# Kernel tuning notes

Measured on AMD Instinct MI355X. Metric: run time of the kernel, lower is better.

The kernel has to match this reference:

```python
import jax, jax.numpy as jnp
import numpy as np

B, C, H, W = 16, 1536, 32, 32
M = 64      # num_clusters
L = 128     # cluster_dim
G = 256     # token_dim
HID = 512
OT_ITERS = 3
EPS = 1e-6


def setup_inputs() -> dict:
    key = jax.random.key(0)
    ks = jax.random.split(key, 12)
    def w(k, shape, fan_in):
        return jax.random.normal(k, shape, jnp.float32) * (1.0 / np.sqrt(fan_in))
    return {
        'x': jax.random.normal(ks[0], (B, C, H, W), jnp.float32),
        't': jax.random.normal(ks[1], (B, C), jnp.float32),
        # token_features: Linear(C->512), ReLU, Linear(512->G)
        'Wt1': w(ks[2], (HID, C), C), 'bt1': jnp.zeros((HID,), jnp.float32),
        'Wt2': w(ks[3], (G, HID), HID), 'bt2': jnp.zeros((G,), jnp.float32),
        # cluster_features: 1x1 Conv(C->512), ReLU, 1x1 Conv(512->L)
        'Wc1': w(ks[4], (HID, C), C), 'bc1': jnp.zeros((HID,), jnp.float32),
        'Wc2': w(ks[5], (L, HID), HID), 'bc2': jnp.zeros((L,), jnp.float32),
        # score: 1x1 Conv(C->512), ReLU, 1x1 Conv(512->M)
        'Ws1': w(ks[6], (HID, C), C), 'bs1': jnp.zeros((HID,), jnp.float32),
        'Ws2': w(ks[7], (M, HID), HID), 'bs2': jnp.zeros((M,), jnp.float32),
        # temp_predictor: Conv1d(L->1, k=1)
        'Wtp': w(ks[8], (L,), L), 'btp': jnp.zeros((), jnp.float32),
        'dust_bin': jnp.asarray(1.0, jnp.float32),
        'burst_b': jnp.asarray(0.0, jnp.float32),
        'burst_p': jnp.asarray(1.0, jnp.float32),
        'lambda_discount': jnp.asarray(0.5, jnp.float32),
    }


def _log_optimal_transport(scores, alpha, iters):
    # scores: [B, m, n]; alpha: scalar dust-bin logit
    b, m, n = scores.shape
    Z0 = jnp.concatenate([scores, jnp.broadcast_to(alpha, (b, 1, n))], axis=1)  # [B, m+1, n]
    norm = -jnp.log(jnp.asarray(m + n, scores.dtype))
    log_mu = jnp.concatenate([jnp.full((m,), norm, scores.dtype),
                              (jnp.log(jnp.asarray(n, scores.dtype)) + norm)[None]])  # [m+1]
    log_nu = jnp.full((n,), norm, scores.dtype)
    u = jnp.zeros((b, m + 1), scores.dtype)
    v = jnp.zeros((b, n), scores.dtype)
    for _ in range(iters):
        u = log_mu - jax.nn.logsumexp(Z0 + v[:, None, :], axis=2)
        v = log_nu - jax.nn.logsumexp(Z0 + u[:, :, None], axis=1)
    return Z0 + u[:, :, None] + v[:, None, :] - norm


def _l2norm(a, axis):
    return a / jnp.maximum(jnp.linalg.norm(a, axis=axis, keepdims=True), 1e-12)


def _forward(x, t, Wt1, bt1, Wt2, bt2, Wc1, bc1, Wc2, bc2, Ws1, bs1, Ws2, bs2,
             Wtp, btp, dust_bin, burst_b, burst_p, lambda_discount):
    b, c, h, w = x.shape
    n = h * w
    xf = x.reshape(b, c, n)  # [B, C, N] (1x1 convs == per-pixel MLP)
    # cluster features f: [B, L, N]
    h1 = jax.nn.relu(jnp.einsum('bcn,oc->bon', xf, Wc1) + bc1[:, None])
    f = jnp.einsum('bhn,lh->bln', h1, Wc2) + bc2[:, None]
    # assignment scores p: [B, M, N]
    h2 = jax.nn.relu(jnp.einsum('bcn,oc->bon', xf, Ws1) + bs1[:, None])
    p = jnp.einsum('bhn,mh->bmn', h2, Ws2) + bs2[:, None]
    # global token: [B, G]
    tok = jax.nn.relu(t @ Wt1.T + bt1) @ Wt2.T + bt2
    # Sinkhorn OT soft assignment, drop dust bin row
    P = jnp.exp(_log_optimal_transport(p, dust_bin, OT_ITERS))[:, :-1, :]  # [B, M, N]
    # burst-aware weighting
    f_norm = _l2norm(f, axis=1)                                  # [B, L, N]
    T_i = jax.nn.softplus(jnp.einsum('bln,l->bn', f, Wtp) + btp)  # [B, N]
    sim = jnp.einsum('bli,blj->bij', f_norm, f_norm)              # [B, N, N]
    T_avg = (T_i[:, :, None] + T_i[:, None, :]) * 0.5
    burst_w = jax.nn.sigmoid(T_avg * sim + burst_b)
    discount = jnp.clip(jnp.sum(burst_w, axis=-1) ** burst_p, 1e-3, 1e3)  # [B, N]
    lam = jax.nn.sigmoid(lambda_discount)
    P_adj = (1.0 - lam) * P + lam * (P / (discount[:, None, :] + EPS))
    # local aggregation: (f[:, :, None, :] * P[:, None, :, :]).sum(-1) == batched matmul
    agg = jnp.einsum('bln,bmn->blm', f, P_adj)  # [B, L, M]
    agg = _l2norm(agg, axis=1).reshape(b, -1)   # [B, L*M]
    tok_n = _l2norm(tok, axis=-1)
    g = jnp.concatenate([tok_n, agg], axis=-1)  # [B, G + L*M]
    return _l2norm(g, axis=-1)


def reference(x, t, Wt1, bt1, Wt2, bt2, Wc1, bc1, Wc2, bc2, Ws1, bs1, Ws2, bs2,
              Wtp, btp, dust_bin, burst_b, burst_p, lambda_discount):
    return _forward(x, t, Wt1, bt1, Wt2, bt2, Wc1, bc1, Wc2, bc2, Ws1, bs1, Ws2, bs2,
                    Wtp, btp, dust_bin, burst_b, burst_p, lambda_discount)
```

## Files before the change

### kernel.cpp

```cpp
#include <hip/hip_runtime.h>
#include <math.h>

#define B_   16
#define C_   1536
#define N_   1024
#define M_   64
#define L_   128
#define G_   256
#define HID_ 512

typedef __attribute__((ext_vector_type(8))) short short8;
typedef __attribute__((ext_vector_type(4))) float floatx4;

__device__ __forceinline__ unsigned short f2bf_rne(float x) {
    unsigned u = __float_as_uint(x);
    unsigned r = u + 0x7fffu + ((u >> 16) & 1u);
    return (unsigned short)(r >> 16);
}
__device__ __forceinline__ unsigned pack_bf2(float lo, float hi) {
    unsigned a = __float_as_uint(lo) + 0x8000u;
    unsigned b = __float_as_uint(hi) + 0x8000u;
    return (a >> 16) | (b & 0xffff0000u);
}

__device__ __forceinline__ void gl2lds16(const void* g, void* l) {
    __builtin_amdgcn_global_load_lds(
        (const __attribute__((address_space(1))) void*)g,
        (__attribute__((address_space(3))) void*)l, 16, 0, 0);
}

__global__ __launch_bounds__(256) void cast_w_kernel(
    const float* __restrict__ Wc1, const float* __restrict__ Ws1,
    const float* __restrict__ Wc2, const float* __restrict__ Ws2,
    unsigned short* __restrict__ Wbf, unsigned short* __restrict__ W2)
{
    const int T1 = 1024 * 1536;
    int idx = blockIdx.x * 256 + threadIdx.x;
    if (idx < T1) {
        float v = (idx < 512 * 1536) ? Wc1[idx] : Ws1[idx - 512 * 1536];
        Wbf[idx] = f2bf_rne(v);
    } else if (idx < T1 + 192 * 1024) {
        int i2 = idx - T1;
        int row = i2 >> 10, k = i2 & 1023;
        float v = 0.f;
        if (row < 128) { if (k < 512) v = Wc2[row * 512 + k]; }
        else           { if (k >= 512) v = Ws2[(row - 128) * 512 + (k - 512)]; }
        W2[i2] = f2bf_rne(v);
    }
}

__global__ __launch_bounds__(256) void xt_kernel(
    const float* __restrict__ x, unsigned short* __restrict__ xT)
{
    __shared__ float Xs[64][65];
    const int t = threadIdx.x;
    const int n0 = blockIdx.x * 64, c0 = blockIdx.y * 64, b = blockIdx.z;
    const float* xb = x + (long)b * C_ * N_;
    #pragma unroll
    for (int it = 0; it < 16; ++it) {
        int idx = it * 256 + t, cr = idx >> 6, nc = idx & 63;
        Xs[cr][nc] = xb[(long)(c0 + cr) * N_ + n0 + nc];
    }
    __syncthreads();
    unsigned* xo = (unsigned*)(xT + (long)b * N_ * C_);
    #pragma unroll
    for (int it = 0; it < 8; ++it) {
        int idx = it * 256 + t, nr = idx >> 5, pc = idx & 31;
        xo[(long)(n0 + nr) * 768 + (c0 >> 1) + pc] =
            pack_bf2(Xs[2 * pc][nr], Xs[2 * pc + 1][nr]);
    }
}

__global__ __launch_bounds__(256, 2) void gemm1_kernel(
    const unsigned short* __restrict__ Wbf, const unsigned short* __restrict__ xT,
    const float* __restrict__ bc1, const float* __restrict__ bs1,
    unsigned short* __restrict__ hT)
{
    __shared__ unsigned short As[128 * 32];
    __shared__ unsigned short Bs[128 * 32];
    const int t = threadIdx.x;
    const int lane = t & 63, w = t >> 6;
    const int n0 = blockIdx.x * 128, o0 = blockIdx.y * 128, b = blockIdx.z;
    const unsigned short* xb = xT + (long)b * N_ * C_;

    const int wo = (w >> 1) * 64, wn = (w & 1) * 64;
    const int lrow = lane & 15, kgrp = lane >> 4;
    const int arow = t >> 2, acol = (t & 3) * 8;

    floatx4 acc[4][4];
    #pragma unroll
    for (int i = 0; i < 4; ++i)
        #pragma unroll
        for (int j = 0; j < 4; ++j) acc[i][j] = (floatx4)0.0f;

    for (int k0 = 0; k0 < C_; k0 += 32) {
        #pragma unroll
        for (int r = 0; r < 2; ++r)
            gl2lds16(Wbf + (long)(o0 + r * 64 + arow) * C_ + k0 + acol,
                     (char*)As + r * 4096 + t * 16);
        #pragma unroll
        for (int r = 0; r < 2; ++r)
            gl2lds16(xb + (long)(n0 + r * 64 + arow) * C_ + k0 + acol,
                     (char*)Bs + r * 4096 + t * 16);
        __syncthreads();
        short8 af[4], bfr[4];
        #pragma unroll
        for (int i = 0; i < 4; ++i)
            af[i] = *(const short8*)((const char*)As +
                        (wo + i * 16 + lrow) * 64 + kgrp * 16);
        #pragma unroll
        for (int j = 0; j < 4; ++j)
            bfr[j] = *(const short8*)((const char*)Bs +
                        (wn + j * 16 + lrow) * 64 + kgrp * 16);
        #pragma unroll
        for (int i = 0; i < 4; ++i)
            #pragma unroll
            for (int j = 0; j < 4; ++j)
                acc[i][j] = __builtin_amdgcn_mfma_f32_16x16x32_bf16(
                    af[i], bfr[j], acc[i][j], 0, 0, 0);
        __syncthreads();
    }

    const float* bias = (o0 < 512) ? bc1 : bs1;
    const int ob = (o0 < 512) ? o0 : o0 - 512;
    #pragma unroll
    for (int i = 0; i < 4; ++i) {
        int orow = wo + i * 16 + kgrp * 4;
        float b0 = bias[ob + orow + 0], b1 = bias[ob + orow + 1];
        float b2 = bias[ob + orow + 2], b3 = bias[ob + orow + 3];
        #pragma unroll
        for (int j = 0; j < 4; ++j) {
            int n = n0 + wn + j * 16 + lrow;
            float v0 = fmaxf(acc[i][j][0] + b0, 0.f);
            float v1 = fmaxf(acc[i][j][1] + b1, 0.f);
            float v2 = fmaxf(acc[i][j][2] + b2, 0.f);
            float v3 = fmaxf(acc[i][j][3] + b3, 0.f);
            uint2 pk;
            pk.x = ((unsigned)f2bf_rne(v0)) | (((unsigned)f2bf_rne(v1)) << 16);
            pk.y = ((unsigned)f2bf_rne(v2)) | (((unsigned)f2bf_rne(v3)) << 16);
            *(uint2*)&hT[((long)b * N_ + n) * 1024 + o0 + orow] = pk;
        }
    }
}

__global__ __launch_bounds__(256, 2) void gemm23_kernel(
    const unsigned short* __restrict__ W2, const unsigned short* __restrict__ hT,
    const float* __restrict__ bc2, const float* __restrict__ bs2,
    float* __restrict__ f, float* __restrict__ p)
{
    __shared__ unsigned short As[64 * 32];
    __shared__ unsigned short Bs[128 * 32];
    const int t = threadIdx.x;
    const int lane = t & 63, w = t >> 6;
    const int n0 = blockIdx.x * 128, o0 = blockIdx.y * 64, b = blockIdx.z;
    const unsigned short* hTb = hT + (long)b * N_ * 1024;

    const int wo = (w >> 1) * 32, wn = (w & 1) * 64;
    const int lrow = lane & 15, kgrp = lane >> 4;
    const int arow = t >> 2, acol = (t & 3) * 8;

    floatx4 acc[2][4];
    #pragma unroll
    for (int i = 0; i < 2; ++i)
        #pragma unroll
        for (int j = 0; j < 4; ++j) acc[i][j] = (floatx4)0.0f;

    for (int k0 = 0; k0 < 1024; k0 += 32) {
        gl2lds16(W2 + (long)(o0 + arow) * 1024 + k0 + acol, (char*)As + t * 16);
        #pragma unroll
        for (int r = 0; r < 2; ++r)
            gl2lds16(hTb + (long)(n0 + r * 64 + arow) * 1024 + k0 + acol,
                     (char*)Bs + r * 4096 + t * 16);
        __syncthreads();
        short8 af[2], bfr[4];
        #pragma unroll
        for (int i = 0; i < 2; ++i)
            af[i] = *(const short8*)((const char*)As +
                        (wo + i * 16 + lrow) * 64 + kgrp * 16);
        #pragma unroll
        for (int j = 0; j < 4; ++j)
            bfr[j] = *(const short8*)((const char*)Bs +
                        (wn + j * 16 + lrow) * 64 + kgrp * 16);
        #pragma unroll
        for (int i = 0; i < 2; ++i)
            #pragma unroll
            for (int j = 0; j < 4; ++j)
                acc[i][j] = __builtin_amdgcn_mfma_f32_16x16x32_bf16(
                    af[i], bfr[j], acc[i][j], 0, 0, 0);
        __syncthreads();
    }

    #pragma unroll
    for (int i = 0; i < 2; ++i) {
        int o = o0 + wo + i * 16 + kgrp * 4;
        #pragma unroll
        for (int j = 0; j < 4; ++j) {
            int n = n0 + wn + j * 16 + lrow;
            #pragma unroll
            for (int r = 0; r < 4; ++r) {
                int oo = o + r;
                float v = acc[i][j][r];
                if (oo < 128) f[((long)b * L_ + oo) * N_ + n] = v + bc2[oo];
                else p[((long)b * M_ + (oo - 128)) * N_ + n] = v + bs2[oo - 128];
            }
        }
    }
}

__global__ __launch_bounds__(256) void token1_kernel(
    const float* __restrict__ t_in, const float* __restrict__ Wt1,
    const float* __restrict__ bt1, float* __restrict__ hid)
{
    const int lane = threadIdx.x & 63, w = threadIdx.x >> 6;
    const int o = blockIdx.x * 4 + w, b = blockIdx.y;
    const float4* wr = (const float4*)(Wt1 + (long)o * C_);
    const float4* tb = (const float4*)(t_in + (long)b * C_);
    float acc = 0.f;
    #pragma unroll
    for (int i = 0; i < 6; ++i) {
        float4 a = wr[i * 64 + lane], tv = tb[i * 64 + lane];
        acc += a.x * tv.x + a.y * tv.y + a.z * tv.z + a.w * tv.w;
    }
    #pragma unroll
    for (int off = 1; off < 64; off <<= 1) acc += __shfl_xor(acc, off);
    if (lane == 0) hid[b * HID_ + o] = fmaxf(acc + bt1[o], 0.f);
}

__global__ __launch_bounds__(256) void token2_kernel(
    const float* __restrict__ hid, const float* __restrict__ Wt2,
    const float* __restrict__ bt2, float* __restrict__ tok)
{
    const int lane = threadIdx.x & 63, w = threadIdx.x >> 6;
    const int g = blockIdx.x * 4 + w, b = blockIdx.y;
    const float4* wr = (const float4*)(Wt2 + (long)g * HID_);
    const float4* hb = (const float4*)(hid + (long)b * HID_);
    float acc = 0.f;
    #pragma unroll
    for (int i = 0; i < 2; ++i) {
        float4 a = wr[i * 64 + lane], hv = hb[i * 64 + lane];
        acc += a.x * hv.x + a.y * hv.y + a.z * hv.z + a.w * hv.w;
    }
    #pragma unroll
    for (int off = 1; off < 64; off <<= 1) acc += __shfl_xor(acc, off);
    if (lane == 0) tok[b * G_ + g] = acc + bt2[g];
}

__global__ __launch_bounds__(256) void token3_kernel(
    const float* __restrict__ tok, float* __restrict__ tokn)
{
    __shared__ float red[4];
    const int b = blockIdx.x, t = threadIdx.x;
    float v = tok[b * G_ + t];
    float ss = v * v;
    #pragma unroll
    for (int off = 1; off < 64; off <<= 1) ss += __shfl_xor(ss, off);
    if ((t & 63) == 0) red[t >> 6] = ss;
    __syncthreads();
    float inv = 1.f / fmaxf(sqrtf(red[0] + red[1] + red[2] + red[3]), 1e-12f);
    tokn[b * G_ + t] = v * inv;
}

template<bool FIRST>
__global__ __launch_bounds__(256) void ku_kernel(
    float* __restrict__ p, const float* __restrict__ dust,
    const float* __restrict__ bvec, float* __restrict__ avec)
{
    const int t = threadIdx.x, lane = t & 63, w = t >> 6;
    const int m = blockIdx.x * 4 + w, b = blockIdx.y;
    if (m > M_) return;
    const float* bv = bvec + b * N_;
    float s = 0.f;
    if (m < M_) {
        float* row = p + ((long)b * M_ + m) * N_;
        #pragma unroll
        for (int i = 0; i < 16; ++i) {
            int n = i * 64 + lane;
            if (FIRST) {
                float K = expf(row[n]);
                row[n] = K;
                s += K;
            } else {
                s += row[n] * bv[n];
            }
        }
    } else {
        float ea = expf(dust[0]);
        if (FIRST) s = 16.f * ea;
        else {
            #pragma unroll
            for (int i = 0; i < 16; ++i) s += bv[i * 64 + lane];
            s *= ea;
        }
    }
    #pragma unroll
    for (int off = 1; off < 64; off <<= 1) s += __shfl_xor(s, off);
    if (lane == 0) {
        float mu = (m < M_) ? (1.f / 1088.f) : (1024.f / 1088.f);
        avec[b * (M_ + 1) + m] = mu / s;
    }
}

__global__ __launch_bounds__(256) void kv_kernel(
    const float* __restrict__ K, const float* __restrict__ dust,
    const float* __restrict__ avec, float* __restrict__ bvec)
{
    __shared__ float a_s[M_ + 1];
    const int t = threadIdx.x, b = blockIdx.y;
    const int n = blockIdx.x * 256 + t;
    if (t < M_ + 1) a_s[t] = avec[b * (M_ + 1) + t];
    __syncthreads();
    float s = expf(dust[0]) * a_s[M_];
    const float* col = K + (long)b * M_ * N_ + n;
    #pragma unroll
    for (int m = 0; m < M_; ++m) s = fmaf(col[(long)m * N_], a_s[m], s);
    bvec[b * N_ + n] = (1.f / 1088.f) / s;
}

__global__ __launch_bounds__(256) void tnorm_kernel(
    const float* __restrict__ f, const float* __restrict__ Wtp,
    const float* __restrict__ btp, unsigned short* __restrict__ fnT,
    float* __restrict__ T, float* __restrict__ draw)
{
    __shared__ float Ft[L_][65];
    __shared__ float invs[64];
    __shared__ float wtp_s[L_];
    const int b = blockIdx.y, n0 = blockIdx.x * 64, t = threadIdx.x;
    const float* fb = f + (long)b * L_ * N_;

    if (t < L_) wtp_s[t] = Wtp[t];
    for (int it = 0; it < 32; ++it) {
        int idx = it * 256 + t;
        int l = idx >> 6, c = idx & 63;
        Ft[l][c] = fb[(long)l * N_ + n0 + c];
    }
    __syncthreads();
    if (t < 64) {
        float ss = 0.f, dot = 0.f;
        #pragma unroll
        for (int l = 0; l < L_; ++l) {
            float v = Ft[l][t];
            ss = fmaf(v, v, ss);
            dot = fmaf(v, wtp_s[l], dot);
        }
        invs[t] = 1.f / fmaxf(sqrtf(ss), 1e-12f);
        float xx = dot + btp[0];
        T[b * N_ + n0 + t] = (xx > 0.f) ? (xx + log1pf(expf(-xx)))
                                        : log1pf(expf(xx));
        draw[b * N_ + n0 + t] = 0.f;
    }
    __syncthreads();
    unsigned* fo = (unsigned*)fnT;
    for (int it = 0; it < 16; ++it) {
        int idx = it * 256 + t;
        int nl = idx >> 6, jp = idx & 63;
        float inv = invs[nl];
        fo[(((long)b * N_ + n0 + nl) << 6) + jp] =
            pack_bf2(Ft[2 * jp][nl] * inv, Ft[2 * jp + 1][nl] * inv);
    }
}

__global__ __launch_bounds__(256) void sim_kernel(
    const unsigned short* __restrict__ fnT, const float* __restrict__ T,
    const float* __restrict__ bb, float* __restrict__ draw)
{
    __shared__ unsigned short As[64 * 136];
    __shared__ unsigned short Bs[64 * 136];
    __shared__ float Ti[64], Tj[64];
    const int b = blockIdx.z, i0 = blockIdx.y * 64, j0base = blockIdx.x * 256;
    const int t = threadIdx.x, lane = t & 63, w = t >> 6;
    const int lrow = lane & 15, kgrp = lane >> 4;
    const unsigned short* fb = fnT + (long)b * N_ * 128;
    const float burstb = bb[0];

    if (t < 64) Ti[t] = T[b * N_ + i0 + t];
    const int srow = t >> 4, scol = (t & 15) * 8;
    #pragma unroll
    for (int r = 0; r < 4; ++r) {
        uint4 av = *(const uint4*)(fb + (long)(i0 + r * 16 + srow) * 128 + scol);
        *(uint4*)((char*)As + (r * 16 + srow) * 272 + scol * 2) = av;
    }

    float rs[4] = {0.f, 0.f, 0.f, 0.f};
    for (int jj = 0; jj < 4; ++jj) {
        const int j0 = j0base + jj * 64;
        __syncthreads();
        #pragma unroll
        for (int r = 0; r < 4; ++r) {
            uint4 bv = *(const uint4*)(fb + (long)(j0 + r * 16 + srow) * 128 + scol);
            *(uint4*)((char*)Bs + (r * 16 + srow) * 272 + scol * 2) = bv;
        }
        if (t >= 64 && t < 128) Tj[t - 64] = T[b * N_ + j0 + (t - 64)];
        __syncthreads();

        floatx4 acc[4];
        #pragma unroll
        for (int j = 0; j < 4; ++j) acc[j] = (floatx4)0.0f;
        #pragma unroll
        for (int k0 = 0; k0 < 128; k0 += 32) {
            short8 af = *(const short8*)((const char*)As +
                            (w * 16 + lrow) * 272 + k0 * 2 + kgrp * 16);
            #pragma unroll
            for (int j = 0; j < 4; ++j) {
                short8 bf = *(const short8*)((const char*)Bs +
                                (j * 16 + lrow) * 272 + k0 * 2 + kgrp * 16);
                acc[j] = __builtin_amdgcn_mfma_f32_16x16x32_bf16(af, bf, acc[j], 0, 0, 0);
            }
        }
        #pragma unroll
        for (int j = 0; j < 4; ++j) {
            float Tjv = Tj[j * 16 + lrow];
            #pragma unroll
            for (int r = 0; r < 4; ++r) {
                float Tiv = Ti[w * 16 + kgrp * 4 + r];
                float xarg = 0.5f * (Tiv + Tjv) * acc[j][r] + burstb;
                rs[r] += 1.f / (1.f + expf(-xarg));
            }
        }
    }

    #pragma unroll
    for (int off = 1; off < 16; off <<= 1)
        #pragma unroll
        for (int r = 0; r < 4; ++r) rs[r] += __shfl_xor(rs[r], off);
    if (lrow == 0) {
        #pragma unroll
        for (int r = 0; r < 4; ++r)
            atomicAdd(&draw[b * N_ + i0 + w * 16 + kgrp * 4 + r], rs[r]);
    }
}

__global__ __launch_bounds__(256) void wn_kernel(
    const float* __restrict__ draw, const float* __restrict__ bp,
    const float* __restrict__ lamd, float* __restrict__ wn,
    float* __restrict__ agg)
{
    const int id = blockIdx.x * 256 + threadIdx.x;
    float d = powf(draw[id], bp[0]);
    d = fminf(fmaxf(d, 1e-3f), 1e3f);
    float lam = 1.f / (1.f + expf(-lamd[0]));
    wn[id] = (1.f - lam) + lam / (d + 1e-6f);
    for (int i = id; i < B_ * L_ * M_; i += B_ * N_) agg[i] = 0.f;
}

__global__ __launch_bounds__(256) void agg_kernel(
    const float* __restrict__ f, const float* __restrict__ Kmat,
    const float* __restrict__ avec, const float* __restrict__ dust,
    const float* __restrict__ wn, float* __restrict__ agg)
{
    __shared__ float fch[L_][65];
    __shared__ float Pch[M_][65];
    __shared__ float a_s[M_ + 1], cf[64];
    const int b = blockIdx.y, n0 = blockIdx.x * 64;
    const int t = threadIdx.x, tx = t & 15, ty = t >> 4;
    const float* fb = f + (long)b * L_ * N_;
    const float* Kb = Kmat + (long)b * M_ * N_;

    if (t < M_ + 1) a_s[t] = avec[b * (M_ + 1) + t];
    __syncthreads();

    for (int idx = t; idx < L_ * 64; idx += 256) {
        int l = idx >> 6, c = idx & 63;
        fch[l][c] = fb[(long)l * N_ + n0 + c];
    }
    for (int idx = t; idx < M_ * 64; idx += 256) {
        int m = idx >> 6, c = idx & 63;
        Pch[m][c] = Kb[(long)m * N_ + n0 + c] * a_s[m];
    }
    __syncthreads();

    if (t < 64) {
        float s = expf(dust[0]) * a_s[M_];
        #pragma unroll
        for (int m = 0; m < M_; ++m) s += Pch[m][t];
        cf[t] = wn[b * N_ + n0 + t] / s;
    }
    __syncthreads();

    float acc[8][4] = {};
    for (int n = 0; n < 64; ++n) {
        float cfn = cf[n];
        float fv[8], pv[4];
        #pragma unroll
        for (int i = 0; i < 8; ++i) fv[i] = fch[ty + 16 * i][n];
        #pragma unroll
        for (int j = 0; j < 4; ++j) pv[j] = Pch[tx * 4 + j][n] * cfn;
        #pragma unroll
        for (int i = 0; i < 8; ++i)
            #pragma unroll
            for (int j = 0; j < 4; ++j)
                acc[i][j] = fmaf(fv[i], pv[j], acc[i][j]);
    }
    #pragma unroll
    for (int i = 0; i < 8; ++i)
        #pragma unroll
        for (int j = 0; j < 4; ++j)
            atomicAdd(&agg[((long)b * L_ + (ty + 16 * i)) * M_ + tx * 4 + j],
                      acc[i][j]);
}

__global__ __launch_bounds__(256) void final_kernel(
    const float* __restrict__ tokn, const float* __restrict__ agg,
    float* __restrict__ out)
{
    __shared__ float invm[M_];
    __shared__ float red[4];
    __shared__ float s_invtot;
    const int b = blockIdx.x, t = threadIdx.x;
    const float* ab = agg + (long)b * L_ * M_;

    if (t < 64) {
        float ss = 0.f;
        for (int l = 0; l < L_; ++l) {
            float v = ab[l * M_ + t];
            ss = fmaf(v, v, ss);
        }
        invm[t] = 1.f / fmaxf(sqrtf(ss), 1e-12f);
    }
    __syncthreads();

    float part;
    {
        float tn = tokn[b * G_ + t];
        part = tn * tn;
    }
    for (int idx = t; idx < L_ * M_; idx += 256) {
        float v = ab[idx] * invm[idx & 63];
        part = fmaf(v, v, part);
    }
    for (int off = 32; off; off >>= 1) part += __shfl_down(part, off);
    if ((t & 63) == 0) red[t >> 6] = part;
    __syncthreads();
    if (t == 0)
        s_invtot = 1.f / fmaxf(sqrtf(red[0] + red[1] + red[2] + red[3]), 1e-12f);
    __syncthreads();

    const float invtot = s_invtot;
    float* ob = out + (long)b * (G_ + L_ * M_);
    ob[t] = tokn[b * G_ + t] * invtot;
    for (int idx = t; idx < L_ * M_; idx += 256)
        ob[G_ + idx] = ab[idx] * invm[idx & 63] * invtot;
}

extern "C" void kernel_launch(void* const* d_in, const int* in_sizes, int n_in,
                              void* d_out, int out_size, void* d_ws, size_t ws_size,
                              hipStream_t stream)
{
    const float* x    = (const float*)d_in[0];
    const float* t_in = (const float*)d_in[1];
    const float* Wt1  = (const float*)d_in[2];
    const float* bt1  = (const float*)d_in[3];
    const float* Wt2  = (const float*)d_in[4];
    const float* bt2  = (const float*)d_in[5];
    const float* Wc1  = (const float*)d_in[6];
    const float* bc1  = (const float*)d_in[7];
    const float* Wc2  = (const float*)d_in[8];
    const float* bc2  = (const float*)d_in[9];
    const float* Ws1  = (const float*)d_in[10];
    const float* bs1  = (const float*)d_in[11];
    const float* Ws2  = (const float*)d_in[12];
    const float* bs2  = (const float*)d_in[13];
    const float* Wtp  = (const float*)d_in[14];
    const float* btp  = (const float*)d_in[15];
    const float* dust = (const float*)d_in[16];
    const float* bb   = (const float*)d_in[17];
    const float* bp   = (const float*)d_in[18];
    const float* lamd = (const float*)d_in[19];

    char* wsb = (char*)d_ws;
    unsigned short* xT  = (unsigned short*)wsb;
    float* f    = (float*)(wsb + 0);
    float* p    = (float*)(wsb + 8388608);
    unsigned short* fnT = (unsigned short*)(wsb + 12582912);
    float* hid  = (float*)(wsb + 16777216);
    float* tok  = (float*)(wsb + 16809984);
    float* tokn = (float*)(wsb + 16826368);
    float* T    = (float*)(wsb + 16842752);
    float* draw = (float*)(wsb + 16908288);
    float* wgt  = (float*)(wsb + 16973824);
    float* agg  = (float*)(wsb + 17039360);
    float* avec = (float*)(wsb + 17563648);
    float* bvec = (float*)(wsb + 17567808);
    unsigned short* hT  = (unsigned short*)(wsb + 50331648);
    unsigned short* Wbf = (unsigned short*)(wsb + 83886080);
    unsigned short* W2  = (unsigned short*)(wsb + 87031808);
    float* out  = (float*)d_out;

    cast_w_kernel<<<6912, 256, 0, stream>>>(Wc1, Ws1, Wc2, Ws2, Wbf, W2);

    xt_kernel   <<<dim3(16, 24, 16), 256, 0, stream>>>(x, xT);
    gemm1_kernel<<<dim3(8, 8, 16), 256, 0, stream>>>(Wbf, xT, bc1, bs1, hT);
    gemm23_kernel<<<dim3(8, 3, 16), 256, 0, stream>>>(W2, hT, bc2, bs2, f, p);

    token1_kernel<<<dim3(128, 16), 256, 0, stream>>>(t_in, Wt1, bt1, hid);
    token2_kernel<<<dim3(64, 16), 256, 0, stream>>>(hid, Wt2, bt2, tok);
    token3_kernel<<<16, 256, 0, stream>>>(tok, tokn);

    ku_kernel<true> <<<dim3(17, 16), 256, 0, stream>>>(p, dust, bvec, avec);
    kv_kernel       <<<dim3(4, 16), 256, 0, stream>>>(p, dust, avec, bvec);
    ku_kernel<false><<<dim3(17, 16), 256, 0, stream>>>(p, dust, bvec, avec);
    kv_kernel       <<<dim3(4, 16), 256, 0, stream>>>(p, dust, avec, bvec);
    ku_kernel<false><<<dim3(17, 16), 256, 0, stream>>>(p, dust, bvec, avec);

    tnorm_kernel<<<dim3(16, 16), 256, 0, stream>>>(f, Wtp, btp, fnT, T, draw);
    sim_kernel  <<<dim3(4, 16, 16), 256, 0, stream>>>(fnT, T, bb, draw);
    wn_kernel   <<<64, 256, 0, stream>>>(draw, bp, lamd, wgt, agg);
    agg_kernel  <<<dim3(16, 16), 256, 0, stream>>>(f, p, avec, dust, wgt, agg);
    final_kernel<<<16, 256, 0, stream>>>(tokn, agg, out);
}
```

Baseline: 392.0 us.

## Rewrite gemm1 as 256x256-tile, 8-wave, double-buffered swizzled-LDS pipeline

After: 376.4 us. 4.0% less time.

```diff
diff --git a/kernel.cpp b/kernel.cpp
--- a/kernel.cpp
+++ b/kernel.cpp
@@ -71,70 +71,116 @@
     }
 }
 
-__global__ __launch_bounds__(256, 2) void gemm1_kernel(
+#define G1_STAGE_A(kt, q)                                                    \
+    gl2lds16(aSrc + (long)(q) * (32 * C_) + (kt) * 64,                       \
+             (char*)g1lds + (((kt) & 1) * 65536 + (q) * 8192) + sdst)
+#define G1_STAGE_B(kt, q)                                                    \
+    gl2lds16(bSrc + (long)(q) * (32 * C_) + (kt) * 64,                       \
+             (char*)g1lds + (((kt) & 1) * 65536 + 32768 + (q) * 8192) + sdst)
+
+#define G1_PHASE(q, STAGES, TAIL)                                            \
+  {                                                                          \
+    const char* ab = cb + aFB + (q) * 8192;                                  \
+    short8 a0 = *(const short8*)(ab + ks0);                                  \
+    short8 a1 = *(const short8*)(ab + ks1);                                  \
+    short8 a2 = *(const short8*)(ab + 2048 + ks0);                           \
+    short8 a3 = *(const short8*)(ab + 2048 + ks1);                           \
+    STAGES                                                                   \
+    __builtin_amdgcn_s_barrier();                                            \
+    asm volatile("s_waitcnt lgkmcnt(0)" ::: "memory");                       \
+    __builtin_amdgcn_sched_barrier(0);                                       \
+    __builtin_amdgcn_s_setprio(1);                                           \
+    _Pragma("unroll")                                                        \
+    for (int fj = 0; fj < 4; ++fj) {                                         \
+      acc[2*(q)][fj]   = __builtin_amdgcn_mfma_f32_16x16x32_bf16(            \
+          a0, bfr[fj][0], acc[2*(q)][fj], 0, 0, 0);                          \
+      acc[2*(q)][fj]   = __builtin_amdgcn_mfma_f32_16x16x32_bf16(            \
+          a1, bfr[fj][1], acc[2*(q)][fj], 0, 0, 0);                          \
+      acc[2*(q)+1][fj] = __builtin_amdgcn_mfma_f32_16x16x32_bf16(            \
+          a2, bfr[fj][0], acc[2*(q)+1][fj], 0, 0, 0);                        \
+      acc[2*(q)+1][fj] = __builtin_amdgcn_mfma_f32_16x16x32_bf16(            \
+          a3, bfr[fj][1], acc[2*(q)+1][fj], 0, 0, 0);                        \
+    }                                                                        \
+    __builtin_amdgcn_s_setprio(0);                                           \
+    TAIL                                                                     \
+    __builtin_amdgcn_s_barrier();                                            \
+    __builtin_amdgcn_sched_barrier(0);                                       \
+  }
+
+#define G1_TILE(tt, S1, S2, TAIL3)                                           \
+  {                                                                          \
+    const char* cb = (const char*)g1lds + ((tt) & 1) * 65536;                \
+    _Pragma("unroll")                                                        \
+    for (int fj = 0; fj < 4; ++fj) {                                         \
+      const char* bb = cb + bFB + (fj >> 1) * 8192 + (fj & 1) * 2048;        \
+      bfr[fj][0] = *(const short8*)(bb + ks0);                               \
+      bfr[fj][1] = *(const short8*)(bb + ks1);                               \
+    }                                                                        \
+    G1_PHASE(0, if (S1) { G1_STAGE_A((tt)+1, 2); G1_STAGE_A((tt)+1, 3); }, ) \
+    G1_PHASE(1, if (S2) { G1_STAGE_B((tt)+2, 0); G1_STAGE_B((tt)+2, 1); }, ) \
+    G1_PHASE(2, if (S2) { G1_STAGE_B((tt)+2, 2); G1_STAGE_B((tt)+2, 3); }, ) \
+    G1_PHASE(3, if (S2) { G1_STAGE_A((tt)+2, 0); G1_STAGE_A((tt)+2, 1); }, TAIL3) \
+  }
+
+__global__ __launch_bounds__(512, 2) void gemm1_kernel(
     const unsigned short* __restrict__ Wbf, const unsigned short* __restrict__ xT,
     const float* __restrict__ bc1, const float* __restrict__ bs1,
     unsigned short* __restrict__ hT)
 {
-    __shared__ unsigned short As[128 * 32];
-    __shared__ unsigned short Bs[128 * 32];
+    __shared__ unsigned short g1lds[65536];
     const int t = threadIdx.x;
     const int lane = t & 63, w = t >> 6;
-    const int n0 = blockIdx.x * 128, o0 = blockIdx.y * 128, b = blockIdx.z;
-    const unsigned short* xb = xT + (long)b * N_ * C_;
-
-    const int wo = (w >> 1) * 64, wn = (w & 1) * 64;
+    const int n0 = blockIdx.x * 256, o0 = blockIdx.y * 256, b = blockIdx.z;
+
+    const int sgrow = ((t & 256) ? 128 : 0) + ((t >> 3) & 31);
+    const int sdst  = t * 16;
+    const int sslot = ((t & 7) ^ ((t >> 3) & 7)) * 8;
+    const unsigned short* aSrc = Wbf + (long)(o0 + sgrow) * C_ + sslot;
+    const unsigned short* bSrc = xT + (long)b * N_ * C_
+                               + (long)(n0 + sgrow) * C_ + sslot;
+
     const int lrow = lane & 15, kgrp = lane >> 4;
-    const int arow = t >> 2, acol = (t & 3) * 8;
-
-    floatx4 acc[4][4];
-    #pragma unroll
-    for (int i = 0; i < 4; ++i)
+    const int wo = (w >> 2) * 128, wn = (w & 3) * 64;
+    const int aFB = (w >> 2) * 4096 + lrow * 128;
+    const int bFB = 32768 + ((w >> 1) & 1) * 4096 + (w & 1) * 16384 + lrow * 128;
+    const int ks0 = (kgrp ^ (lrow & 7)) * 16;
+    const int ks1 = ((4 + kgrp) ^ (lrow & 7)) * 16;
+
+    floatx4 acc[8][4];
+    #pragma unroll
+    for (int i = 0; i < 8; ++i)
         #pragma unroll
         for (int j = 0; j < 4; ++j) acc[i][j] = (floatx4)0.0f;
-
-    for (int k0 = 0; k0 < C_; k0 += 32) {
-        #pragma unroll
-        for (int r = 0; r < 2; ++r)
-            gl2lds16(Wbf + (long)(o0 + r * 64 + arow) * C_ + k0 + acol,
-                     (char*)As + r * 4096 + t * 16);
-        #pragma unroll
-        for (int r = 0; r < 2; ++r)
-            gl2lds16(xb + (long)(n0 + r * 64 + arow) * C_ + k0 + acol,
-                     (char*)Bs + r * 4096 + t * 16);
-        __syncthreads();
-        short8 af[4], bfr[4];
-        #pragma unroll
-        for (int i = 0; i < 4; ++i)
-            af[i] = *(const short8*)((const char*)As +
-                        (wo + i * 16 + lrow) * 64 + kgrp * 16);
-        #pragma unroll
-        for (int j = 0; j < 4; ++j)
-            bfr[j] = *(const short8*)((const char*)Bs +
-                        (wn + j * 16 + lrow) * 64 + kgrp * 16);
-        #pragma unroll
-        for (int i = 0; i < 4; ++i)
-            #pragma unroll
-            for (int j = 0; j < 4; ++j)
-                acc[i][j] = __builtin_amdgcn_mfma_f32_16x16x32_bf16(
-                    af[i], bfr[j], acc[i][j], 0, 0, 0);
-        __syncthreads();
-    }
+    short8 bfr[4][2];
+
+    #pragma unroll
+    for (int q = 0; q < 4; ++q) { G1_STAGE_A(0, q); G1_STAGE_B(0, q); }
+    #pragma unroll
+    for (int q = 0; q < 4; ++q) G1_STAGE_B(1, q);
+    G1_STAGE_A(1, 0); G1_STAGE_A(1, 1);
+    asm volatile("s_waitcnt vmcnt(6)" ::: "memory");
+    __builtin_amdgcn_s_barrier();
+    __builtin_amdgcn_sched_barrier(0);
+
+    #pragma unroll 2
+    for (int t8 = 0; t8 < 22; ++t8)
+        G1_TILE(t8, 1, 1, asm volatile("s_waitcnt vmcnt(6)" ::: "memory");)
+    G1_TILE(22, 1, 0, asm volatile("s_waitcnt vmcnt(0)" ::: "memory");)
+    G1_TILE(23, 0, 0, )
 
     const float* bias = (o0 < 512) ? bc1 : bs1;
     const int ob = (o0 < 512) ? o0 : o0 - 512;
     #pragma unroll
-    for (int i = 0; i < 4; ++i) {
-        int orow = wo + i * 16 + kgrp * 4;
-        float b0 = bias[ob + orow + 0], b1 = bias[ob + orow + 1];
-        float b2 = bias[ob + orow + 2], b3 = bias[ob + orow + 3];
-        #pragma unroll
-        for (int j = 0; j < 4; ++j) {
-            int n = n0 + wn + j * 16 + lrow;
-            float v0 = fmaxf(acc[i][j][0] + b0, 0.f);
-            float v1 = fmaxf(acc[i][j][1] + b1, 0.f);
-            float v2 = fmaxf(acc[i][j][2] + b2, 0.f);
-            float v3 = fmaxf(acc[i][j][3] + b3, 0.f);
+    for (int fi = 0; fi < 8; ++fi) {
+        const int orow = wo + fi * 16 + kgrp * 4;
+        float4 bv = *(const float4*)&bias[ob + orow];
+        #pragma unroll
+        for (int fj = 0; fj < 4; ++fj) {
+            const int n = n0 + wn + fj * 16 + lrow;
+            float v0 = fmaxf(acc[fi][fj][0] + bv.x, 0.f);
+            float v1 = fmaxf(acc[fi][fj][1] + bv.y, 0.f);
+            float v2 = fmaxf(acc[fi][fj][2] + bv.z, 0.f);
+            float v3 = fmaxf(acc[fi][fj][3] + bv.w, 0.f);
             uint2 pk;
             pk.x = ((unsigned)f2bf_rne(v0)) | (((unsigned)f2bf_rne(v1)) << 16);
             pk.y = ((unsigned)f2bf_rne(v2)) | (((unsigned)f2bf_rne(v3)) << 16);
@@ -588,7 +634,7 @@
     cast_w_kernel<<<6912, 256, 0, stream>>>(Wc1, Ws1, Wc2, Ws2, Wbf, W2);
 
     xt_kernel   <<<dim3(16, 24, 16), 256, 0, stream>>>(x, xT);
-    gemm1_kernel<<<dim3(8, 8, 16), 256, 0, stream>>>(Wbf, xT, bc1, bs1, hT);
+    gemm1_kernel<<<dim3(4, 4, 16), 512, 0, stream>>>(Wbf, xT, bc1, bs1, hT);
     gemm23_kernel<<<dim3(8, 3, 16), 256, 0, stream>>>(W2, hT, bc2, bs2, f, p);
 
     token1_kernel<<<dim3(128, 16), 256, 0, stream>>>(t_in, Wt1, bt1, hid);
```
